# Kernel tuning notes

Measured on AMD Instinct MI355X. Metric: run time of the kernel, lower is better.

The kernel has to match this reference:

```python
import jax, jax.numpy as jnp
import numpy as np
import math

IN_CH = 1024
OUT_CH = 1024
QK_DIM = 512
NHEADS = 8
NDIM = QK_DIM // NHEADS  # 64 per-head qk dim
VDIM = OUT_CH // NHEADS  # 128 per-head value dim
SCALE = 1.0 / math.sqrt(NDIM)


def setup_inputs() -> dict:
    key = jax.random.key(0)
    ks = jax.random.split(key, 7)
    B, N = 4, 2048
    x = jax.random.normal(ks[0], (B, N, IN_CH), dtype=jnp.float32)
    # Linear weights stored as [in, out] so y = x @ W + b
    s_in = 1.0 / math.sqrt(IN_CH)
    Wq = jax.random.uniform(ks[1], (IN_CH, QK_DIM), jnp.float32, -s_in, s_in)
    bq = jax.random.uniform(ks[2], (QK_DIM,), jnp.float32, -s_in, s_in)
    Wk = jax.random.uniform(ks[3], (IN_CH, QK_DIM), jnp.float32, -s_in, s_in)
    bk = jax.random.uniform(ks[4], (QK_DIM,), jnp.float32, -s_in, s_in)
    Wv = jax.random.uniform(ks[5], (IN_CH, OUT_CH), jnp.float32, -s_in, s_in)
    bv = jax.random.uniform(ks[6], (OUT_CH,), jnp.float32, -s_in, s_in)
    return {"x": x, "Wq": Wq, "bq": bq, "Wk": Wk, "bk": bk, "Wv": Wv, "bv": bv}


def reference(x, Wq, bq, Wk, bk, Wv, bv):
    B, N, C = x.shape
    Q = (x @ Wq + bq).reshape(B, N, NHEADS, NDIM)
    K = (x @ Wk + bk).reshape(B, N, NHEADS, NDIM)
    V = (x @ Wv + bv).reshape(B, N, NHEADS, VDIM)
    # scores: [B, H, N, N]
    scores = jnp.einsum("bnhd,bmhd->bhnm", Q, K) * SCALE
    attn = jax.nn.softmax(scores, axis=-1)
    # message: [B, N, H, VDIM] -> [B, N, OUT_CH]
    msg = jnp.einsum("bhnm,bmhv->bnhv", attn, V)
    return msg.reshape(B, N, OUT_CH)
```

## Files before the change

### kernel.cpp

```cpp
#include <hip/hip_runtime.h>
#include <hip/hip_bf16.h>
#include <math.h>


using bf16 = __hip_bfloat16;
typedef __attribute__((ext_vector_type(8))) short short8;
typedef __attribute__((ext_vector_type(4))) short bf16x4;
typedef __attribute__((ext_vector_type(4))) float f32x4;

#define SCALE_F 0.125f
#define LOG2E   1.44269504088896f

#if defined(__HIP_DEVICE_COMPILE__)
  #if __has_builtin(__builtin_amdgcn_mfma_f32_16x16x16bf16_1k)
    #define MFMA_PV(a,b,c) __builtin_amdgcn_mfma_f32_16x16x16bf16_1k(a,b,c,0,0,0)
  #else
    #define MFMA_PV(a,b,c) __builtin_amdgcn_mfma_f32_16x16x16_bf16(a,b,c,0,0,0)
  #endif
#else
  #define MFMA_PV(a,b,c) (c)
#endif

__device__ __forceinline__ void async_ld16(const void* g, void* l) {
  __builtin_amdgcn_global_load_lds(
      (const __attribute__((address_space(1))) unsigned int*)g,
      (__attribute__((address_space(3))) unsigned int*)l, 16, 0, 0);
}

__global__ __launch_bounds__(256) void convert_x(const float* __restrict__ x,
                                                 bf16* __restrict__ xb)
{
  const int i = (blockIdx.x * 256 + threadIdx.x) * 8;
  const float4 a = *(const float4*)(x + i);
  const float4 b = *(const float4*)(x + i + 4);
  union { bf16 h[8]; short8 s; } u;
  u.h[0] = __float2bfloat16(a.x); u.h[1] = __float2bfloat16(a.y);
  u.h[2] = __float2bfloat16(a.z); u.h[3] = __float2bfloat16(a.w);
  u.h[4] = __float2bfloat16(b.x); u.h[5] = __float2bfloat16(b.y);
  u.h[6] = __float2bfloat16(b.z); u.h[7] = __float2bfloat16(b.w);
  *(short8*)(xb + i) = u.s;
}

__global__ __launch_bounds__(256) void transpose_weights(
    const float* __restrict__ Wq, const float* __restrict__ Wk,
    const float* __restrict__ Wv, bf16* __restrict__ Wt)
{
  __shared__ __align__(16) bf16 t[32][33];
  const int i0 = blockIdx.x * 32;
  const int o0 = blockIdx.y * 32;
  const int tx = threadIdx.x & 31, ty = threadIdx.x >> 5;
#pragma unroll
  for (int s = 0; s < 32; s += 8) {
    const int i = i0 + ty + s;
    const int o = o0 + tx;
    const float w = (o < 512)  ? Wq[(size_t)i * 512 + o]
                  : (o < 1024) ? Wk[(size_t)i * 512 + (o - 512)]
                               : Wv[(size_t)i * 1024 + (o - 1024)];
    t[ty + s][tx] = __float2bfloat16(w);
  }
  __syncthreads();
#pragma unroll
  for (int s = 0; s < 32; s += 8)
    Wt[(size_t)(o0 + ty + s) * 1024 + i0 + tx] = t[tx][ty + s];
}

__global__ __launch_bounds__(256, 2) void qkv_gemm(
    const bf16* __restrict__ xb, const bf16* __restrict__ Wt,
    const float* __restrict__ bq, const float* __restrict__ bk,
    const float* __restrict__ bv, bf16* __restrict__ QKV)
{
  __shared__ __align__(16) bf16 As[128 * 64];
  __shared__ __align__(16) bf16 Bs[128 * 64];
  const int tid = threadIdx.x;
  const int w = tid >> 6, lane = tid & 63, quad = lane >> 4, l16 = lane & 15;
  const int m0 = blockIdx.y * 128, n0 = blockIdx.x * 128;
  const int wm = (w >> 1) * 64, wn = (w & 1) * 64;
  f32x4 acc[4][4];
  const f32x4 z4 = {0.f, 0.f, 0.f, 0.f};
#pragma unroll
  for (int mi = 0; mi < 4; ++mi)
#pragma unroll
    for (int ni = 0; ni < 4; ++ni) acc[mi][ni] = z4;

  for (int k0 = 0; k0 < 1024; k0 += 64) {
    __syncthreads();
#pragma unroll
    for (int it = 0; it < 4; ++it) {
      const int L = it * 256 + tid;
      const int row = L >> 3;
      const int c16 = (L & 7) ^ (row & 7);
      async_ld16(xb + (size_t)(m0 + row) * 1024 + k0 + c16 * 8, &As[L * 8]);
      async_ld16(Wt + (size_t)(n0 + row) * 1024 + k0 + c16 * 8, &Bs[L * 8]);
    }
    __syncthreads();
#pragma unroll
    for (int kk = 0; kk < 2; ++kk) {
      short8 af[4], bfr[4];
#pragma unroll
      for (int mi = 0; mi < 4; ++mi) {
        const int row = wm + mi * 16 + l16;
        const int p = ((kk << 2) | quad) ^ (row & 7);
        af[mi] = *(const short8*)&As[row * 64 + p * 8];
      }
#pragma unroll
      for (int ni = 0; ni < 4; ++ni) {
        const int row = wn + ni * 16 + l16;
        const int p = ((kk << 2) | quad) ^ (row & 7);
        bfr[ni] = *(const short8*)&Bs[row * 64 + p * 8];
      }
#pragma unroll
      for (int mi = 0; mi < 4; ++mi)
#pragma unroll
        for (int ni = 0; ni < 4; ++ni)
          acc[mi][ni] = __builtin_amdgcn_mfma_f32_16x16x32_bf16(af[mi], bfr[ni], acc[mi][ni], 0, 0, 0);
    }
  }
#pragma unroll
  for (int ni = 0; ni < 4; ++ni) {
    const int colg = n0 + wn + ni * 16 + l16;
    const float bias = colg < 512 ? bq[colg]
                     : (colg < 1024 ? bk[colg - 512] : bv[colg - 1024]);
#pragma unroll
    for (int mi = 0; mi < 4; ++mi)
#pragma unroll
      for (int reg = 0; reg < 4; ++reg) {
        const int rowg = m0 + wm + mi * 16 + quad * 4 + reg;
        QKV[(size_t)rowg * 2048 + colg] = __float2bfloat16(acc[mi][ni][reg] + bias);
      }
  }
}

__global__ __launch_bounds__(256) void transpose_v(
    const bf16* __restrict__ QKV, bf16* __restrict__ Vt)
{
  __shared__ __align__(16) bf16 t[32][33];
  const int r0 = blockIdx.x * 32;
  const int c0 = blockIdx.y * 32;
  const int tx = threadIdx.x & 31, ty = threadIdx.x >> 5;
#pragma unroll
  for (int s = 0; s < 32; s += 8)
    t[ty + s][tx] = QKV[(size_t)(r0 + ty + s) * 2048 + 1024 + c0 + tx];
  __syncthreads();
#pragma unroll
  for (int s = 0; s < 32; s += 8)
    Vt[(size_t)(c0 + ty + s) * 8192 + r0 + tx] = t[tx][ty + s];
}

__global__ __launch_bounds__(512, 4) void flash_attn(
    const bf16* __restrict__ QKV, const bf16* __restrict__ Vt, float* __restrict__ out)
{
  __shared__ __align__(16) bf16 Qs[128 * 64];
  __shared__ __align__(16) bf16 Ks[128 * 64];
  __shared__ __align__(16) bf16 Vs[128 * 128];
  const int tid = threadIdx.x;
  const int w = tid >> 6, lane = tid & 63, quad = lane >> 4, l16 = lane & 15;
  const int q0 = blockIdx.x * 128;
  const int h  = blockIdx.y;
  const size_t tb = (size_t)blockIdx.z * 2048;

#pragma unroll
  for (int it = 0; it < 2; ++it) {
    const int L = it * 512 + tid;
    const int row = L >> 3;
    const int c16 = (L & 7) ^ (row & 7);
    async_ld16(QKV + (tb + q0 + row) * 2048 + h * 64 + c16 * 8, &Qs[L * 8]);
  }
  __syncthreads();

  short8 aq[2];
#pragma unroll
  for (int kk = 0; kk < 2; ++kk) {
    const int row = w * 16 + l16;
    const int p = ((kk << 2) | quad) ^ (row & 7);
    aq[kk] = *(const short8*)&Qs[row * 64 + p * 8];
  }

  f32x4 O[8];
  const f32x4 z4 = {0.f, 0.f, 0.f, 0.f};
#pragma unroll
  for (int t = 0; t < 8; ++t) O[t] = z4;
  float m_run = -1e30f, l_run = 0.f;
  const float c2 = SCALE_F * LOG2E;

  for (int k0 = 0; k0 < 2048; k0 += 128) {
    __syncthreads();
#pragma unroll
    for (int it = 0; it < 2; ++it) {
      const int L = it * 512 + tid;
      const int row = L >> 3;
      const int c16 = (L & 7) ^ (row & 7);
      async_ld16(QKV + (tb + k0 + row) * 2048 + 512 + h * 64 + c16 * 8, &Ks[L * 8]);
    }
#pragma unroll
    for (int it = 0; it < 4; ++it) {
      const int L = it * 512 + tid;
      const int row = L >> 4;
      const int c16 = (L & 15) ^ (row & 15);
      async_ld16(Vt + (size_t)(h * 128 + row) * 8192 + tb + k0 + c16 * 8, &Vs[L * 8]);
    }
    __syncthreads();

    f32x4 S[8];
#pragma unroll
    for (int kt = 0; kt < 8; ++kt) {
      S[kt] = z4;
#pragma unroll
      for (int kk = 0; kk < 2; ++kk) {
        const int row = kt * 16 + l16;
        const int p = ((kk << 2) | quad) ^ (row & 7);
        const short8 ak = *(const short8*)&Ks[row * 64 + p * 8];
        S[kt] = __builtin_amdgcn_mfma_f32_16x16x32_bf16(ak, aq[kk], S[kt], 0, 0, 0);
      }
    }

    float mloc = S[0][0];
#pragma unroll
    for (int kt = 0; kt < 8; ++kt)
#pragma unroll
      for (int r = 0; r < 4; ++r) mloc = fmaxf(mloc, S[kt][r]);
    mloc = fmaxf(mloc, __shfl_xor(mloc, 16, 64));
    mloc = fmaxf(mloc, __shfl_xor(mloc, 32, 64));
    const float mnew = fmaxf(m_run, mloc);
    const float alpha = exp2f((m_run - mnew) * c2);
    float rsum = 0.f;
    bf16x4 P[8];
#pragma unroll
    for (int kt = 0; kt < 8; ++kt) {
      union { bf16 h[4]; bf16x4 s; } up;
#pragma unroll
      for (int r = 0; r < 4; ++r) {
        const float pv = exp2f((S[kt][r] - mnew) * c2);
        rsum += pv;
        up.h[r] = __float2bfloat16(pv);
      }
      P[kt] = up.s;
    }
    rsum += __shfl_xor(rsum, 16, 64);
    rsum += __shfl_xor(rsum, 32, 64);
    l_run = l_run * alpha + rsum;
    m_run = mnew;
#pragma unroll
    for (int t = 0; t < 8; ++t) {
      O[t][0] *= alpha; O[t][1] *= alpha; O[t][2] *= alpha; O[t][3] *= alpha;
    }

#pragma unroll
    for (int kt = 0; kt < 8; ++kt) {
#pragma unroll
      for (int vt = 0; vt < 8; ++vt) {
        const int vrow = vt * 16 + l16;
        const int s = (2 * kt + (quad >> 1)) ^ l16;
        const bf16x4 av = *(const bf16x4*)((const char*)Vs + vrow * 256 + s * 16 + (quad & 1) * 8);
        O[vt] = MFMA_PV(av, P[kt], O[vt]);
      }
    }
  }

  const float inv_l = 1.0f / l_run;
  const size_t qg = tb + q0 + w * 16 + l16;
#pragma unroll
  for (int vt = 0; vt < 8; ++vt) {
    float4 st;
    st.x = O[vt][0] * inv_l; st.y = O[vt][1] * inv_l;
    st.z = O[vt][2] * inv_l; st.w = O[vt][3] * inv_l;
    *(float4*)(out + qg * 1024 + h * 128 + vt * 16 + quad * 4) = st;
  }
}

extern "C" void kernel_launch(void* const* d_in, const int* in_sizes, int n_in,
                              void* d_out, int out_size, void* d_ws, size_t ws_size,
                              hipStream_t stream) {
  const float* x  = (const float*)d_in[0];
  const float* Wq = (const float*)d_in[1];
  const float* bq = (const float*)d_in[2];
  const float* Wk = (const float*)d_in[3];
  const float* bk = (const float*)d_in[4];
  const float* Wv = (const float*)d_in[5];
  const float* bv = (const float*)d_in[6];
  float* out = (float*)d_out;

  char* ws = (char*)d_ws;
  bf16* QKV = (bf16*)ws;
  bf16* Vt  = (bf16*)(ws + 33554432);
  bf16* Wt  = (bf16*)(ws + 33554432 + 16777216);
  bf16* xb  = (bf16*)(ws + 33554432 + 16777216 + 4194304);

  convert_x<<<dim3(4096), 256, 0, stream>>>(x, xb);
  transpose_weights<<<dim3(32, 64), 256, 0, stream>>>(Wq, Wk, Wv, Wt);
  qkv_gemm<<<dim3(16, 64), 256, 0, stream>>>(xb, Wt, bq, bk, bv, QKV);
  transpose_v<<<dim3(256, 32), 256, 0, stream>>>(QKV, Vt);
  flash_attn<<<dim3(16, 8, 4), 512, 0, stream>>>(QKV, Vt, out);
}
```

Baseline: 257.1 us.

## Switch flash attention to 32x32x16 MFMA with 4 waves of 32 query rows

Rewrites the attention kernel to use 32x32x16 bf16 MFMA tiles, with each of 4 waves owning 32 query rows instead of 8 waves owning 16. P fragments are rearranged across half-waves with shuffles to feed the PV matmul, and the output is transposed through shared memory so global stores are coalesced. The aim is higher MFMA throughput and fewer LDS reads per FLOP. The cost is more register pressure from the 16-wide accumulators, fewer threads per block, and extra synchronisation in the epilogue.

```diff
diff --git a/kernel.cpp b/kernel.cpp
--- a/kernel.cpp
+++ b/kernel.cpp
@@ -5,21 +5,11 @@
 
 using bf16 = __hip_bfloat16;
 typedef __attribute__((ext_vector_type(8))) short short8;
-typedef __attribute__((ext_vector_type(4))) short bf16x4;
 typedef __attribute__((ext_vector_type(4))) float f32x4;
+typedef __attribute__((ext_vector_type(16))) float f32x16;
 
 #define SCALE_F 0.125f
 #define LOG2E   1.44269504088896f
-
-#if defined(__HIP_DEVICE_COMPILE__)
-  #if __has_builtin(__builtin_amdgcn_mfma_f32_16x16x16bf16_1k)
-    #define MFMA_PV(a,b,c) __builtin_amdgcn_mfma_f32_16x16x16bf16_1k(a,b,c,0,0,0)
-  #else
-    #define MFMA_PV(a,b,c) __builtin_amdgcn_mfma_f32_16x16x16_bf16(a,b,c,0,0,0)
-  #endif
-#else
-  #define MFMA_PV(a,b,c) (c)
-#endif
 
 __device__ __forceinline__ void async_ld16(const void* g, void* l) {
   __builtin_amdgcn_global_load_lds(
@@ -146,124 +136,148 @@
     Vt[(size_t)(c0 + ty + s) * 8192 + r0 + tx] = t[tx][ty + s];
 }
 
-__global__ __launch_bounds__(512, 4) void flash_attn(
+__global__ __launch_bounds__(256, 2) void flash_attn(
     const bf16* __restrict__ QKV, const bf16* __restrict__ Vt, float* __restrict__ out)
 {
-  __shared__ __align__(16) bf16 Qs[128 * 64];
-  __shared__ __align__(16) bf16 Ks[128 * 64];
-  __shared__ __align__(16) bf16 Vs[128 * 128];
+  __shared__ __align__(16) bf16 smem[128 * 64 + 128 * 64 + 128 * 128];
+  bf16* Qs = smem;
+  bf16* Ks = smem + 128 * 64;
+  bf16* Vs = smem + 2 * 128 * 64;
   const int tid = threadIdx.x;
-  const int w = tid >> 6, lane = tid & 63, quad = lane >> 4, l16 = lane & 15;
+  const int w = tid >> 6, lane = tid & 63, l31 = lane & 31, hi = lane >> 5;
   const int q0 = blockIdx.x * 128;
   const int h  = blockIdx.y;
   const size_t tb = (size_t)blockIdx.z * 2048;
 
 #pragma unroll
-  for (int it = 0; it < 2; ++it) {
-    const int L = it * 512 + tid;
+  for (int it = 0; it < 4; ++it) {
+    const int L = it * 256 + tid;
     const int row = L >> 3;
     const int c16 = (L & 7) ^ (row & 7);
     async_ld16(QKV + (tb + q0 + row) * 2048 + h * 64 + c16 * 8, &Qs[L * 8]);
   }
   __syncthreads();
 
-  short8 aq[2];
-#pragma unroll
-  for (int kk = 0; kk < 2; ++kk) {
-    const int row = w * 16 + l16;
-    const int p = ((kk << 2) | quad) ^ (row & 7);
-    aq[kk] = *(const short8*)&Qs[row * 64 + p * 8];
-  }
-
-  f32x4 O[8];
-  const f32x4 z4 = {0.f, 0.f, 0.f, 0.f};
-#pragma unroll
-  for (int t = 0; t < 8; ++t) O[t] = z4;
+  short8 qf[4];
+  const int qrow = w * 32 + l31;
+#pragma unroll
+  for (int d = 0; d < 4; ++d) {
+    const int p = (2 * d + hi) ^ (qrow & 7);
+    qf[d] = *(const short8*)&Qs[qrow * 64 + p * 8];
+  }
+
+  f32x16 O[4];
+#pragma unroll
+  for (int t = 0; t < 4; ++t)
+#pragma unroll
+    for (int e = 0; e < 16; ++e) O[t][e] = 0.f;
   float m_run = -1e30f, l_run = 0.f;
   const float c2 = SCALE_F * LOG2E;
 
   for (int k0 = 0; k0 < 2048; k0 += 128) {
     __syncthreads();
 #pragma unroll
-    for (int it = 0; it < 2; ++it) {
-      const int L = it * 512 + tid;
+    for (int it = 0; it < 4; ++it) {
+      const int L = it * 256 + tid;
       const int row = L >> 3;
       const int c16 = (L & 7) ^ (row & 7);
       async_ld16(QKV + (tb + k0 + row) * 2048 + 512 + h * 64 + c16 * 8, &Ks[L * 8]);
     }
 #pragma unroll
-    for (int it = 0; it < 4; ++it) {
-      const int L = it * 512 + tid;
+    for (int it = 0; it < 8; ++it) {
+      const int L = it * 256 + tid;
       const int row = L >> 4;
       const int c16 = (L & 15) ^ (row & 15);
       async_ld16(Vt + (size_t)(h * 128 + row) * 8192 + tb + k0 + c16 * 8, &Vs[L * 8]);
     }
     __syncthreads();
 
-    f32x4 S[8];
-#pragma unroll
-    for (int kt = 0; kt < 8; ++kt) {
-      S[kt] = z4;
-#pragma unroll
-      for (int kk = 0; kk < 2; ++kk) {
-        const int row = kt * 16 + l16;
-        const int p = ((kk << 2) | quad) ^ (row & 7);
-        const short8 ak = *(const short8*)&Ks[row * 64 + p * 8];
-        S[kt] = __builtin_amdgcn_mfma_f32_16x16x32_bf16(ak, aq[kk], S[kt], 0, 0, 0);
+    f32x16 S[4];
+#pragma unroll
+    for (int kt = 0; kt < 4; ++kt) {
+#pragma unroll
+      for (int e = 0; e < 16; ++e) S[kt][e] = 0.f;
+      const int krow = kt * 32 + l31;
+#pragma unroll
+      for (int d = 0; d < 4; ++d) {
+        const int p = (2 * d + hi) ^ (krow & 7);
+        const short8 kf = *(const short8*)&Ks[krow * 64 + p * 8];
+        S[kt] = __builtin_amdgcn_mfma_f32_32x32x16_bf16(kf, qf[d], S[kt], 0, 0, 0);
       }
     }
 
     float mloc = S[0][0];
 #pragma unroll
-    for (int kt = 0; kt < 8; ++kt)
-#pragma unroll
-      for (int r = 0; r < 4; ++r) mloc = fmaxf(mloc, S[kt][r]);
-    mloc = fmaxf(mloc, __shfl_xor(mloc, 16, 64));
+    for (int kt = 0; kt < 4; ++kt)
+#pragma unroll
+      for (int e = 0; e < 16; ++e) mloc = fmaxf(mloc, S[kt][e]);
     mloc = fmaxf(mloc, __shfl_xor(mloc, 32, 64));
     const float mnew = fmaxf(m_run, mloc);
     const float alpha = exp2f((m_run - mnew) * c2);
     float rsum = 0.f;
-    bf16x4 P[8];
-#pragma unroll
-    for (int kt = 0; kt < 8; ++kt) {
-      union { bf16 h[4]; bf16x4 s; } up;
-#pragma unroll
-      for (int r = 0; r < 4; ++r) {
-        const float pv = exp2f((S[kt][r] - mnew) * c2);
-        rsum += pv;
-        up.h[r] = __float2bfloat16(pv);
-      }
-      P[kt] = up.s;
-    }
-    rsum += __shfl_xor(rsum, 16, 64);
+    unsigned int pk[4][8];
+#pragma unroll
+    for (int kt = 0; kt < 4; ++kt)
+#pragma unroll
+      for (int dw = 0; dw < 8; ++dw) {
+        const float p0 = exp2f((S[kt][2 * dw]     - mnew) * c2);
+        const float p1 = exp2f((S[kt][2 * dw + 1] - mnew) * c2);
+        rsum += p0 + p1;
+        union { bf16 hh[2]; unsigned int u; } cc;
+        cc.hh[0] = __float2bfloat16(p0); cc.hh[1] = __float2bfloat16(p1);
+        pk[kt][dw] = cc.u;
+      }
     rsum += __shfl_xor(rsum, 32, 64);
     l_run = l_run * alpha + rsum;
     m_run = mnew;
 #pragma unroll
-    for (int t = 0; t < 8; ++t) {
-      O[t][0] *= alpha; O[t][1] *= alpha; O[t][2] *= alpha; O[t][3] *= alpha;
-    }
-
-#pragma unroll
-    for (int kt = 0; kt < 8; ++kt) {
-#pragma unroll
-      for (int vt = 0; vt < 8; ++vt) {
-        const int vrow = vt * 16 + l16;
-        const int s = (2 * kt + (quad >> 1)) ^ l16;
-        const bf16x4 av = *(const bf16x4*)((const char*)Vs + vrow * 256 + s * 16 + (quad & 1) * 8);
-        O[vt] = MFMA_PV(av, P[kt], O[vt]);
+    for (int t = 0; t < 4; ++t)
+#pragma unroll
+      for (int e = 0; e < 16; ++e) O[t][e] *= alpha;
+
+#pragma unroll
+    for (int c16 = 0; c16 < 8; ++c16) {
+      const int kt = c16 >> 1, b4 = (c16 & 1) * 4;
+      const unsigned int lo0 = pk[kt][b4],     lo1 = pk[kt][b4 + 1];
+      const unsigned int up0 = pk[kt][b4 + 2], up1 = pk[kt][b4 + 3];
+      const unsigned int s0 = hi ? lo0 : up0, s1 = hi ? lo1 : up1;
+      const unsigned int r0 = (unsigned int)__shfl_xor((int)s0, 32, 64);
+      const unsigned int r1 = (unsigned int)__shfl_xor((int)s1, 32, 64);
+      union { unsigned int d[4]; short8 v; } pf;
+      pf.d[0] = hi ? r0 : lo0;  pf.d[1] = hi ? r1 : lo1;
+      pf.d[2] = hi ? up0 : r0;  pf.d[3] = hi ? up1 : r1;
+#pragma unroll
+      for (int vt = 0; vt < 4; ++vt) {
+        const int vrow = vt * 32 + l31;
+        const int p = (2 * c16 + hi) ^ (vrow & 15);
+        const short8 vf = *(const short8*)&Vs[vrow * 128 + p * 8];
+        O[vt] = __builtin_amdgcn_mfma_f32_32x32x16_bf16(vf, pf.v, O[vt], 0, 0, 0);
       }
     }
   }
 
   const float inv_l = 1.0f / l_run;
-  const size_t qg = tb + q0 + w * 16 + l16;
-#pragma unroll
-  for (int vt = 0; vt < 8; ++vt) {
-    float4 st;
-    st.x = O[vt][0] * inv_l; st.y = O[vt][1] * inv_l;
-    st.z = O[vt][2] * inv_l; st.w = O[vt][3] * inv_l;
-    *(float4*)(out + qg * 1024 + h * 128 + vt * 16 + quad * 4) = st;
+  float* tbuf = (float*)smem;
+  const int qg = tid >> 1;
+  const int part = tid & 1;
+  for (int vt = 0; vt < 4; ++vt) {
+    __syncthreads();
+#pragma unroll
+    for (int e = 0; e < 16; ++e) {
+      const int vl = (e & 3) + 8 * (e >> 2) + 4 * hi;
+      tbuf[vl * 132 + w * 32 + l31] = O[vt][e] * inv_l;
+    }
+    __syncthreads();
+    float* dst = out + (tb + q0 + qg) * 1024 + h * 128 + vt * 32 + part * 16;
+#pragma unroll
+    for (int i = 0; i < 4; ++i) {
+      float4 v4;
+      v4.x = tbuf[(part * 16 + 4 * i + 0) * 132 + qg];
+      v4.y = tbuf[(part * 16 + 4 * i + 1) * 132 + qg];
+      v4.z = tbuf[(part * 16 + 4 * i + 2) * 132 + qg];
+      v4.w = tbuf[(part * 16 + 4 * i + 3) * 132 + qg];
+      *(float4*)(dst + 4 * i) = v4;
+    }
   }
 }
 
@@ -289,5 +303,5 @@
   transpose_weights<<<dim3(32, 64), 256, 0, stream>>>(Wq, Wk, Wv, Wt);
   qkv_gemm<<<dim3(16, 64), 256, 0, stream>>>(xb, Wt, bq, bk, bv, QKV);
   transpose_v<<<dim3(256, 32), 256, 0, stream>>>(QKV, Vt);
-  flash_attn<<<dim3(16, 8, 4), 512, 0, stream>>>(QKV, Vt, out);
-}
+  flash_attn<<<dim3(16, 8, 4), 256, 0, stream>>>(QKV, Vt, out);
+}
```

After: 249.3 us. -3.0%, faster.
